# Kernel tuning notes

Measured on AMD Instinct MI355X. Metric: run time of the kernel, lower is better.

The kernel has to match this reference:

```python
import jax, jax.numpy as jnp
import numpy as np

INPUT_SIZE = 64
HIDDEN = 16
BATCH = 1048576


def setup_inputs() -> dict:
    key = jax.random.key(0)
    ks = jax.random.split(key, 16)
    D = INPUT_SIZE + HIDDEN
    s = 1.0 / np.sqrt(D)  # torch nn.Linear default init scale
    inp = {
        "x": jax.random.normal(ks[0], (BATCH, INPUT_SIZE), jnp.float32),
        "h_prev": jax.random.normal(ks[1], (BATCH, HIDDEN), jnp.float32),
        "c_prev": jax.random.normal(ks[2], (BATCH, HIDDEN), jnp.float32),
        "delta_t": jax.random.uniform(ks[3], (BATCH,), jnp.float32),
    }
    names = ["i", "f", "o", "c", "d"]
    for j, n in enumerate(names):
        inp[f"W_{n}"] = jax.random.uniform(ks[4 + 2 * j], (D, HIDDEN), jnp.float32, -s, s)
        inp[f"b_{n}"] = jax.random.uniform(ks[5 + 2 * j], (HIDDEN,), jnp.float32, -s, s)
    return inp


def reference(x, h_prev, c_prev, delta_t, W_i, b_i, W_f, b_f, W_o, b_o, W_c, b_c, W_d, b_d):
    combined = jnp.concatenate([x, h_prev], axis=1)  # [B, D]
    # Fuse the five small GEMMs into one [D, 5H] GEMM (same math).
    W = jnp.concatenate([W_i, W_f, W_o, W_c, W_d], axis=1)  # [D, 5H]
    b = jnp.concatenate([b_i, b_f, b_o, b_c, b_d])  # [5H]
    z = combined @ W + b  # [B, 5H]
    zi, zf, zo, zc, zd = jnp.split(z, 5, axis=1)
    i = jnp.tanh(zi)
    f = jnp.tanh(zf)
    o = jnp.tanh(zo)
    c_tilde = jnp.tanh(zc)
    decay = jax.nn.softplus(zd)
    c_decay = c_prev * jnp.exp(-decay * delta_t[:, None])
    c_next = f * c_decay + i * c_tilde
    h_next = o * jnp.tanh(c_next)
    return (h_next, c_next)
```

## Files before the change

### kernel.cpp

```cpp
#include <hip/hip_runtime.h>


#define BATCH   1048576
#define NTILES  (BATCH / 16)
#define NBLOCKS 8192
#define NWAVES  (NBLOCKS * 4)
#define L2E     1.442695041f
#define LN2     0.6931471806f

typedef __bf16 bf16x8 __attribute__((ext_vector_type(8)));
typedef float  f32x4  __attribute__((ext_vector_type(4)));

#define WS_BIAS_OFF 15360
#define WS_BYTES    15680

__device__ __forceinline__ float fast_tanh(float x) {
    float e = __builtin_amdgcn_exp2f(x * (2.0f * L2E));
    return 1.0f - 2.0f * __builtin_amdgcn_rcpf(e + 1.0f);
}

__global__ void pack_w_kernel(const float* __restrict__ Wi, const float* __restrict__ bi,
                              const float* __restrict__ Wf, const float* __restrict__ bf_,
                              const float* __restrict__ Wo, const float* __restrict__ bo,
                              const float* __restrict__ Wc, const float* __restrict__ bc,
                              const float* __restrict__ Wd, const float* __restrict__ bd,
                              void* __restrict__ ws)
{
    const float* W[5]  = {Wi, Wf, Wo, Wc, Wd};
    const float* BP[5] = {bi, bf_, bo, bc, bd};
    const int b    = blockIdx.x;
    const int lane = threadIdx.x;
    if (b < 15) {
        const int t = b / 3, kt = b % 3;
        const int quad = lane >> 4, col = lane & 15;
        bf16x8 f;
        #pragma unroll
        for (int j = 0; j < 8; ++j) {
            int k = kt * 32 + quad * 8 + j;
            float v = (k < 80) ? W[t][k * 16 + col] : 0.0f;
            f[j] = (__bf16)v;
        }
        ((bf16x8*)ws)[b * 64 + lane] = f;
    } else {
        if (lane < 80) {
            int t = lane >> 4, col = lane & 15;
            ((float*)((char*)ws + WS_BIAS_OFF))[lane] = BP[t][col];
        }
    }
}

__global__ __launch_bounds__(256, 4)
void ctlstm_kernel(const float* __restrict__ x,
                   const float* __restrict__ hprev,
                   const float* __restrict__ cprev,
                   const float* __restrict__ dt,
                   const void* __restrict__ ws,
                   float* __restrict__ out)
{
    __shared__ __align__(16) char smem[WS_BYTES];
    const int tid = threadIdx.x;

    {
        const float4* src = (const float4*)ws;
        float4*       dst = (float4*)smem;
        #pragma unroll
        for (int i = 0; i < 4; ++i) {
            int idx = tid + i * 256;
            if (idx < WS_BYTES / 16) dst[idx] = src[idx];
        }
    }
    __syncthreads();

    const int lane = tid & 63;
    const int col  = lane & 15;
    const int quad = lane >> 4;

    float4 b4[5];
    #pragma unroll
    for (int t = 0; t < 5; ++t)
        b4[t] = *(const float4*)(smem + WS_BIAS_OFF + t * 64 + quad * 16);

    const int gw = (blockIdx.x * 256 + tid) >> 6;

    const float4* X4 = (const float4*)x;
    const float4* H4 = (const float4*)hprev;
    const float4* C4 = (const float4*)cprev;

    const int arow0 = (gw << 4) + col;
    const int arow1 = ((gw + NWAVES) << 4) + col;

    float4 a0 = X4[arow0 * 16 + quad * 2];
    float4 a1 = X4[arow0 * 16 + quad * 2 + 1];
    float4 a2 = X4[arow0 * 16 + quad * 2 + 8];
    float4 a3 = X4[arow0 * 16 + quad * 2 + 9];
    float4 cv0 = C4[arow0 * 4 + quad];
    float  dv0 = dt[arow0];

    float4 g0 = X4[arow1 * 16 + quad * 2];
    float4 g1 = X4[arow1 * 16 + quad * 2 + 1];
    float4 g2 = X4[arow1 * 16 + quad * 2 + 8];
    float4 g3 = X4[arow1 * 16 + quad * 2 + 9];
    float4 cv1 = C4[arow1 * 4 + quad];
    float  dv1 = dt[arow1];

    float4 a4 = make_float4(0.f, 0.f, 0.f, 0.f), a5 = a4;
    float4 g4 = a4, g5 = a4;
    if (quad < 2) {
        a4 = H4[arow0 * 4 + quad * 2];
        a5 = H4[arow0 * 4 + quad * 2 + 1];
        g4 = H4[arow1 * 4 + quad * 2];
        g5 = H4[arow1 * 4 + quad * 2 + 1];
    }

    const bf16x8* WF = (const bf16x8*)smem;

    auto process = [&](int arow,
                       const float4& p0, const float4& p1, const float4& p2,
                       const float4& p3, const float4& p4, const float4& p5,
                       const float4& cp4, float dtv) {
        bf16x8 A0, A1, A2;
        #pragma unroll
        for (int j = 0; j < 4; ++j) {
            A0[j]     = (__bf16)((const float*)&p0)[j];
            A0[j + 4] = (__bf16)((const float*)&p1)[j];
            A1[j]     = (__bf16)((const float*)&p2)[j];
            A1[j + 4] = (__bf16)((const float*)&p3)[j];
            A2[j]     = (__bf16)((const float*)&p4)[j];
            A2[j + 4] = (__bf16)((const float*)&p5)[j];
        }

        f32x4 acc[5];
        #pragma unroll
        for (int t = 0; t < 5; ++t) {
            f32x4 c0 = {b4[t].x, b4[t].y, b4[t].z, b4[t].w};
            c0 = __builtin_amdgcn_mfma_f32_16x16x32_bf16(WF[(t * 3 + 0) * 64 + lane], A0, c0, 0, 0, 0);
            c0 = __builtin_amdgcn_mfma_f32_16x16x32_bf16(WF[(t * 3 + 1) * 64 + lane], A1, c0, 0, 0, 0);
            acc[t] = __builtin_amdgcn_mfma_f32_16x16x32_bf16(WF[(t * 3 + 2) * 64 + lane], A2, c0, 0, 0, 0);
        }

        f32x4 hn4, cn4;
        #pragma unroll
        for (int r = 0; r < 4; ++r) {
            float zi = acc[0][r], zf = acc[1][r], zo = acc[2][r];
            float zc = acc[3][r], zd = acc[4][r];

            float i_g = fast_tanh(zi);
            float f_g = fast_tanh(zf);
            float o_g = fast_tanh(zo);
            float ctl = fast_tanh(zc);

            float ax = fabsf(zd);
            float e  = __builtin_amdgcn_exp2f(-ax * L2E);
            float sp = fmaxf(zd, 0.0f) + __builtin_amdgcn_logf(1.0f + e) * LN2;

            float cdec = ((const float*)&cp4)[r] * __builtin_amdgcn_exp2f(-sp * dtv * L2E);
            float cn   = f_g * cdec + i_g * ctl;
            float hn   = o_g * fast_tanh(cn);

            hn4[r] = hn;
            cn4[r] = cn;
        }
        __builtin_nontemporal_store(hn4, (f32x4*)(out + (size_t)arow * 16 + quad * 4));
        __builtin_nontemporal_store(cn4, (f32x4*)(out + (size_t)BATCH * 16 + (size_t)arow * 16 + quad * 4));
    };

    process(arow0, a0, a1, a2, a3, a4, a5, cv0, dv0);
    process(arow1, g0, g1, g2, g3, g4, g5, cv1, dv1);
}

extern "C" void kernel_launch(void* const* d_in, const int* in_sizes, int n_in,
                              void* d_out, int out_size, void* d_ws, size_t ws_size,
                              hipStream_t stream) {
    pack_w_kernel<<<16, 64, 0, stream>>>(
        (const float*)d_in[4],  (const float*)d_in[5],
        (const float*)d_in[6],  (const float*)d_in[7],
        (const float*)d_in[8],  (const float*)d_in[9],
        (const float*)d_in[10], (const float*)d_in[11],
        (const float*)d_in[12], (const float*)d_in[13],
        d_ws);
    ctlstm_kernel<<<NBLOCKS, 256, 0, stream>>>(
        (const float*)d_in[0], (const float*)d_in[1],
        (const float*)d_in[2], (const float*)d_in[3],
        d_ws, (float*)d_out);
}
```

Measured before the change: 503.7 us.

## Coalesce x/h loads and transpose to MFMA layout through LDS

Each lane now loads x and h_prev with fully contiguous float4 reads instead of the strided per-row fragment pattern. The values are converted to bf16 and written into a per-wave LDS tile with an XOR swizzle, then read back in the MFMA A-operand layout. The aim is better global-load coalescing, at the cost of extra LDS traffic, 10 KB more shared memory per block, and intra-wave LDS ordering with no explicit barrier.

```diff
diff --git a/kernel.cpp b/kernel.cpp
--- a/kernel.cpp
+++ b/kernel.cpp
@@ -2,7 +2,6 @@
 
 
 #define BATCH   1048576
-#define NTILES  (BATCH / 16)
 #define NBLOCKS 8192
 #define NWAVES  (NBLOCKS * 4)
 #define L2E     1.442695041f
@@ -10,6 +9,7 @@
 
 typedef __bf16 bf16x8 __attribute__((ext_vector_type(8)));
 typedef float  f32x4  __attribute__((ext_vector_type(4)));
+typedef unsigned int u32;
 
 #define WS_BIAS_OFF 15360
 #define WS_BYTES    15680
@@ -17,6 +17,13 @@
 __device__ __forceinline__ float fast_tanh(float x) {
     float e = __builtin_amdgcn_exp2f(x * (2.0f * L2E));
     return 1.0f - 2.0f * __builtin_amdgcn_rcpf(e + 1.0f);
+}
+
+__device__ __forceinline__ u32 pkbf(float a, float b) {
+    union { __bf16 h[2]; u32 u; } v;
+    v.h[0] = (__bf16)a;
+    v.h[1] = (__bf16)b;
+    return v.u;
 }
 
 __global__ void pack_w_kernel(const float* __restrict__ Wi, const float* __restrict__ bi,
@@ -58,6 +65,7 @@
                    float* __restrict__ out)
 {
     __shared__ __align__(16) char smem[WS_BYTES];
+    __shared__ __align__(16) u32 tilebuf[4][640];
     const int tid = threadIdx.x;
 
     {
@@ -72,8 +80,10 @@
     __syncthreads();
 
     const int lane = tid & 63;
+    const int wid  = tid >> 6;
     const int col  = lane & 15;
     const int quad = lane >> 4;
+    u32* tb = tilebuf[wid];
 
     float4 b4[5];
     #pragma unroll
@@ -81,53 +91,63 @@
         b4[t] = *(const float4*)(smem + WS_BIAS_OFF + t * 64 + quad * 16);
 
     const int gw = (blockIdx.x * 256 + tid) >> 6;
+    const int T0 = gw, T1 = gw + NWAVES;
+    const int ar0 = (T0 << 4) + col;
+    const int ar1 = (T1 << 4) + col;
 
     const float4* X4 = (const float4*)x;
     const float4* H4 = (const float4*)hprev;
     const float4* C4 = (const float4*)cprev;
 
-    const int arow0 = (gw << 4) + col;
-    const int arow1 = ((gw + NWAVES) << 4) + col;
-
-    float4 a0 = X4[arow0 * 16 + quad * 2];
-    float4 a1 = X4[arow0 * 16 + quad * 2 + 1];
-    float4 a2 = X4[arow0 * 16 + quad * 2 + 8];
-    float4 a3 = X4[arow0 * 16 + quad * 2 + 9];
-    float4 cv0 = C4[arow0 * 4 + quad];
-    float  dv0 = dt[arow0];
-
-    float4 g0 = X4[arow1 * 16 + quad * 2];
-    float4 g1 = X4[arow1 * 16 + quad * 2 + 1];
-    float4 g2 = X4[arow1 * 16 + quad * 2 + 8];
-    float4 g3 = X4[arow1 * 16 + quad * 2 + 9];
-    float4 cv1 = C4[arow1 * 4 + quad];
-    float  dv1 = dt[arow1];
-
-    float4 a4 = make_float4(0.f, 0.f, 0.f, 0.f), a5 = a4;
-    float4 g4 = a4, g5 = a4;
-    if (quad < 2) {
-        a4 = H4[arow0 * 4 + quad * 2];
-        a5 = H4[arow0 * 4 + quad * 2 + 1];
-        g4 = H4[arow1 * 4 + quad * 2];
-        g5 = H4[arow1 * 4 + quad * 2 + 1];
-    }
+    float4 xa[4], xb[4];
+    #pragma unroll
+    for (int L = 0; L < 4; ++L) xa[L] = X4[T0 * 256 + L * 64 + lane];
+    float4 ha  = H4[T0 * 64 + lane];
+    float4 cva = C4[ar0 * 4 + quad];
+    float  dva = dt[ar0];
+    #pragma unroll
+    for (int L = 0; L < 4; ++L) xb[L] = X4[T1 * 256 + L * 64 + lane];
+    float4 hb  = H4[T1 * 64 + lane];
+    float4 cvb = C4[ar1 * 4 + quad];
+    float  dvb = dt[ar1];
+
+    const int wkt = (lane >> 3) & 1;
+    const int wq  = (lane & 7) >> 1;
+    const int wj  = (lane & 1) * 2;
+    const int wrb = lane >> 4;
+    const int hq  = (lane & 3) >> 1;
+    const int hrow = lane >> 2;
+
+    const int swz = (quad & 1) << 2;
+    const int gr0 = (((0 * 4 + quad) * 16 + col) ^ swz) * 4;
+    const int gr1 = (((1 * 4 + quad) * 16 + col) ^ swz) * 4;
+    const int gr2 = 512 + ((quad & 1) * 16 + col) * 4;
 
     const bf16x8* WF = (const bf16x8*)smem;
 
-    auto process = [&](int arow,
-                       const float4& p0, const float4& p1, const float4& p2,
-                       const float4& p3, const float4& p4, const float4& p5,
+    auto process = [&](int arow, const float4* xv, const float4& hv,
                        const float4& cp4, float dtv) {
-        bf16x8 A0, A1, A2;
-        #pragma unroll
-        for (int j = 0; j < 4; ++j) {
-            A0[j]     = (__bf16)((const float*)&p0)[j];
-            A0[j + 4] = (__bf16)((const float*)&p1)[j];
-            A1[j]     = (__bf16)((const float*)&p2)[j];
-            A1[j + 4] = (__bf16)((const float*)&p3)[j];
-            A2[j]     = (__bf16)((const float*)&p4)[j];
-            A2[j + 4] = (__bf16)((const float*)&p5)[j];
-        }
+        #pragma unroll
+        for (int L = 0; L < 4; ++L) {
+            int row = L * 4 + wrb;
+            int g = ((wkt * 4 + wq) * 16 + row) ^ ((wq & 1) << 2);
+            uint2 d;
+            d.x = pkbf(xv[L].x, xv[L].y);
+            d.y = pkbf(xv[L].z, xv[L].w);
+            *(uint2*)&tb[g * 4 + wj] = d;
+        }
+        {
+            uint2 d;
+            d.x = pkbf(hv.x, hv.y);
+            d.y = pkbf(hv.z, hv.w);
+            *(uint2*)&tb[512 + (hq * 16 + hrow) * 4 + wj] = d;
+        }
+
+        bf16x8 A0 = *(const bf16x8*)&tb[gr0];
+        bf16x8 A1 = *(const bf16x8*)&tb[gr1];
+        uint4 a2u = *(const uint4*)&tb[gr2];
+        if (quad >= 2) { a2u.x = 0; a2u.y = 0; a2u.z = 0; a2u.w = 0; }
+        bf16x8 A2 = *(const bf16x8*)&a2u;
 
         f32x4 acc[5];
         #pragma unroll
@@ -164,8 +184,8 @@
         __builtin_nontemporal_store(cn4, (f32x4*)(out + (size_t)BATCH * 16 + (size_t)arow * 16 + quad * 4));
     };
 
-    process(arow0, a0, a1, a2, a3, a4, a5, cv0, dv0);
-    process(arow1, g0, g1, g2, g3, g4, g5, cv1, dv1);
+    process(ar0, xa, ha, cva, dva);
+    process(ar1, xb, hb, cvb, dvb);
 }
 
 extern "C" void kernel_launch(void* const* d_in, const int* in_sizes, int n_in,
```

New measurement: 502.2 us. No clear change (-0.3%).
